# Kernel tuning notes

Measured on AMD Instinct MI355X. Metric: run time of the kernel, lower is better.

## Reference

```python
import jax, jax.numpy as jnp
import numpy as np
from jax.scipy.special import logsumexp

VOCAB, EMB, HID, K = 50000, 256, 512, 48
H = HID // 2
B, T = 64, 512


def setup_inputs() -> dict:
    key = jax.random.key(0)
    ks = jax.random.split(key, 15)
    f = lambda k, s: jax.random.normal(k, s, jnp.float32) * 0.1
    return {
        "x": jax.random.randint(ks[0], (B, T), 0, VOCAB),
        "tags": jax.random.randint(ks[1], (B, T), 0, K),
        "mask": jnp.ones((B, T), jnp.bool_),
        "emb": f(ks[2], (VOCAB, EMB)),
        "Wih_f": f(ks[3], (4 * H, EMB)),
        "Whh_f": f(ks[4], (4 * H, H)),
        "b_f": f(ks[5], (4 * H,)),
        "Wih_b": f(ks[6], (4 * H, EMB)),
        "Whh_b": f(ks[7], (4 * H, H)),
        "b_b": f(ks[8], (4 * H,)),
        "fc_W": f(ks[9], (K, HID)),
        "fc_b": f(ks[10], (K,)),
        "start_t": f(ks[11], (K,)),
        "end_t": f(ks[12], (K,)),
        "trans": f(ks[13], (K, K)),
    }


def _lstm_dir(xs, Wih, Whh, b, reverse):
    # xs: [S, N, E]; scan over axis 0 (PyTorch gate order i,f,g,o; bias = b_ih+b_hh)
    n = xs.shape[1]
    hdim = Whh.shape[1]

    def step(carry, x_t):
        h, c = carry
        gates = x_t @ Wih.T + h @ Whh.T + b
        i, fg, g, o = jnp.split(gates, 4, axis=-1)
        i = jax.nn.sigmoid(i)
        fg = jax.nn.sigmoid(fg)
        g = jnp.tanh(g)
        o = jax.nn.sigmoid(o)
        c = fg * c + i * g
        h = o * jnp.tanh(c)
        return (h, c), h

    init = (jnp.zeros((n, hdim), xs.dtype), jnp.zeros((n, hdim), xs.dtype))
    _, hs = jax.lax.scan(step, init, xs, reverse=reverse)
    return hs


def _crf_nll(emissions, tags, mask, start_t, end_t, trans):
    # torchcrf with batch_first=True, reduction='mean'; returns -llh.mean()
    em = jnp.transpose(emissions, (1, 0, 2))  # [T,B,K] time-major
    tg = tags.T                                # [T,B]
    m = mask.T.astype(em.dtype)                # [T,B]
    bidx = jnp.arange(em.shape[1])

    # numerator: score of the gold tag path
    emit = jnp.take_along_axis(em, tg[..., None], axis=-1)[..., 0]  # [T,B]
    tr = trans[tg[:-1], tg[1:]]                                      # [T-1,B]
    num = start_t[tg[0]] + emit[0] + jnp.sum((tr + emit[1:]) * m[1:], axis=0)
    last = (jnp.sum(mask, axis=1) - 1).astype(jnp.int32)             # [B]
    num = num + end_t[tg[last, bidx]]

    # denominator: forward algorithm (sequential logsumexp recurrence)
    def step(alpha, inp):
        e_t, m_t = inp
        nxt = logsumexp(alpha[:, :, None] + trans[None] + e_t[:, None, :], axis=1)
        return jnp.where(m_t[:, None] > 0, nxt, alpha), None

    alpha0 = start_t + em[0]                     # [B,K]
    alpha, _ = jax.lax.scan(step, alpha0, (em[1:], m[1:]))
    den = logsumexp(alpha + end_t, axis=-1)      # [B]
    return -jnp.mean(num - den)


def reference(x, tags, mask, emb, Wih_f, Whh_f, b_f, Wih_b, Whh_b, b_b, fc_W, fc_b, start_t, end_t, trans):
    table = emb.at[0].set(0.0)  # padding_idx=0 row is zero
    e = table[x]                # [B,T,EMB]
    # Faithful to source: batch-first embeds fed into a seq-first nn.LSTM,
    # so the recurrence runs over axis 0 (the data batch axis).
    h_f = _lstm_dir(e, Wih_f, Whh_f, b_f, False)
    h_b = _lstm_dir(e, Wih_b, Whh_b, b_b, True)
    lstm_out = jnp.concatenate([h_f, h_b], axis=-1)  # [B,T,HID]
    emissions = lstm_out @ fc_W.T + fc_b             # [B,T,K]
    return _crf_nll(emissions, tags, mask, start_t, end_t, trans)
```

## Files before the change

kernel.cpp:

```cpp
#include <hip/hip_runtime.h>
#include <hip/hip_bf16.h>

#define VOCAB 50000
#define EMBD 256
#define HIDD 512
#define KTAG 48
#define HD 256
#define BB 64
#define TT 512
#define GATES 1024

typedef __bf16 bf16x8 __attribute__((ext_vector_type(8)));
typedef float f32x4 __attribute__((ext_vector_type(4)));

#define GLDS16(gp, lp) __builtin_amdgcn_global_load_lds( \
    (const __attribute__((address_space(1))) void*)(gp), \
    (__attribute__((address_space(3))) void*)(lp), 16, 0, 0)

__device__ __forceinline__ f32x4 mfma16(bf16x8 a, bf16x8 b, f32x4 c){
  return __builtin_amdgcn_mfma_f32_16x16x32_bf16(a, b, c, 0, 0, 0);
}
__device__ __forceinline__ float fsig(float x){
  return __builtin_amdgcn_rcpf(1.0f + __expf(-x));
}
__device__ __forceinline__ float ftanh(float x){
  x = fminf(10.0f, fmaxf(-10.0f, x));
  float e = __expf(2.0f*x);
  return (e - 1.0f) * __builtin_amdgcn_rcpf(e + 1.0f);
}

__global__ __launch_bounds__(256) void convert_all(
    const float* emb, const float* wf, const float* wb,
    const float* uf, const float* ub, const float* fc,
    __bf16* o_emb, __bf16* o_wih, __bf16* o_uf, __bf16* o_ub, __bf16* o_fc){
  const long N_emb = (long)VOCAB*EMBD;
  const long N_w   = 1024L*256;
  const long N_fc  = 48L*512;
  const long total = N_emb + 4*N_w + N_fc;
  for (long i = (long)blockIdx.x*256 + threadIdx.x; i < total; i += (long)gridDim.x*256){
    long j = i;
    if (j < N_emb){ o_emb[j] = (__bf16)((j < EMBD) ? 0.0f : emb[j]); continue; }
    j -= N_emb;
    if (j < N_w){ o_wih[j] = (__bf16)wf[j]; continue; }
    j -= N_w;
    if (j < N_w){ o_wih[N_w + j] = (__bf16)wb[j]; continue; }
    j -= N_w;
    if (j < N_w){ o_uf[j] = (__bf16)uf[j]; continue; }
    j -= N_w;
    if (j < N_w){ o_ub[j] = (__bf16)ub[j]; continue; }
    j -= N_w;
    o_fc[j] = (__bf16)fc[j];
  }
}

__global__ __launch_bounds__(256) void gemm_pre(const int* x, const __bf16* embb,
                                                const __bf16* wih, __bf16* pre){
  __shared__ __attribute__((aligned(16))) __bf16 As[128*32];
  __shared__ __attribute__((aligned(16))) __bf16 Bs[128*32];
  const int bid = blockIdx.x;
  const int bm = bid >> 4, bn = bid & 15;
  const int m0 = bm*128, n0 = bn*128;
  const int tid = threadIdx.x, l = tid & 63, w = tid >> 6;
  const int lr = l & 15, lk = l >> 4;
  const int wm = w >> 1, wn = w & 1;
  f32x4 acc[4][4];
  #pragma unroll
  for (int a=0;a<4;a++) for (int b2=0;b2<4;b2++) acc[a][b2] = (f32x4){0.f,0.f,0.f,0.f};

  const __bf16* agp[2];
  const __bf16* bgp[2];
  #pragma unroll
  for (int c=0;c<2;c++){
    const int id = w*2 + c;
    const int slot = id*64 + l;
    const int r = slot >> 2, kk = (slot & 3)*8;
    const int idx = x[m0 + r];
    agp[c] = embb + (size_t)idx*EMBD + kk;
    bgp[c] = wih + (size_t)(n0 + r)*EMBD + kk;
  }

  for (int k0 = 0; k0 < EMBD; k0 += 32){
    __syncthreads();
    #pragma unroll
    for (int c=0;c<2;c++){
      const int id = w*2 + c;
      GLDS16(agp[c] + k0, As + id*512);
      GLDS16(bgp[c] + k0, Bs + id*512);
    }
    asm volatile("s_waitcnt vmcnt(0)" ::: "memory");
    __syncthreads();
    bf16x8 af[4], bfr[4];
    #pragma unroll
    for (int mt=0;mt<4;mt++) af[mt] = *(const bf16x8*)(&As[(wm*64 + mt*16 + lr)*32 + lk*8]);
    #pragma unroll
    for (int nt=0;nt<4;nt++) bfr[nt] = *(const bf16x8*)(&Bs[(wn*64 + nt*16 + lr)*32 + lk*8]);
    #pragma unroll
    for (int mt=0;mt<4;mt++)
      #pragma unroll
      for (int nt=0;nt<4;nt++)
        acc[mt][nt] = mfma16(af[mt], bfr[nt], acc[mt][nt]);
  }
  #pragma unroll
  for (int mt=0;mt<4;mt++)
    #pragma unroll
    for (int nt=0;nt<4;nt++)
      #pragma unroll
      for (int r=0;r<4;r++){
        const int row = m0 + wm*64 + mt*16 + lk*4 + r;
        const int col = n0 + wn*64 + nt*16 + lr;
        pre[(size_t)row*2048 + col] = (__bf16)acc[mt][nt][r];
      }
}

__global__ __launch_bounds__(512, 1) void lstm_rec(const __bf16* pre, const __bf16* whhF,
                                                   const __bf16* whhB, const float* biasF,
                                                   const float* biasB, __bf16* hcat){
  __shared__ __attribute__((aligned(16))) __bf16 hLDS[16*264];
  __shared__ __attribute__((aligned(16))) __bf16 preLDS[2][16*1032];
  const int bid = blockIdx.x;
  const int dir = bid & 1, tg = bid >> 1;
  const int t0 = tg*16;
  const int tid = threadIdx.x, l = tid & 63, w = tid >> 6;
  const int lr = l & 15, lk = l >> 4;
  const __bf16* whh = dir ? whhB : whhF;
  const float* bias = dir ? biasB : biasF;

  bf16x8 Bf[4][2][8];
  #pragma unroll
  for (int q=0;q<4;q++)
    #pragma unroll
    for (int j=0;j<2;j++)
      #pragma unroll
      for (int kt=0;kt<8;kt++){
        const int n = q*256 + w*32 + j*16 + lr;
        Bf[q][j][kt] = *(const bf16x8*)(&whh[(size_t)n*HD + kt*32 + lk*8]);
      }

  float brg[4][2];
  #pragma unroll
  for (int q=0;q<4;q++)
    #pragma unroll
    for (int j=0;j<2;j++)
      brg[q][j] = bias[q*256 + w*32 + j*16 + lr];

  float cst[2][4];
  #pragma unroll
  for (int j=0;j<2;j++)
    #pragma unroll
    for (int r=0;r<4;r++) cst[j][r] = 0.f;

  auto stage = [&](int buf, int bs){
    #pragma unroll
    for (int c2=0;c2<4;c2++){
      const int id = w*4 + c2;
      const int r = id >> 1, half = id & 1;
      const __bf16* g = pre + (size_t)(bs*TT + t0 + r)*2048 + dir*1024 + half*512 + l*8;
      GLDS16(g, &preLDS[buf][r*1032 + half*512]);
    }
  };

  stage(0, dir ? (BB-1) : 0);
  int prev_b = 0;

  #pragma unroll 1
  for (int s = 0; s < BB; s++){
    const int bs = dir ? (BB-1 - s) : s;
    const int buf = s & 1;
    asm volatile("s_waitcnt vmcnt(0)" ::: "memory");
    __syncthreads();
    if (s < BB-1) stage(buf^1, dir ? (BB-2 - s) : (s+1));
    if (s > 0){
      const int row = tid >> 5, ch = tid & 31;
      bf16x8 hv = *(const bf16x8*)(&hLDS[row*264 + ch*8]);
      *(bf16x8*)(&hcat[(size_t)(prev_b*TT + t0 + row)*HIDD + dir*HD + ch*8]) = hv;
    }
    f32x4 acc[4][2];
    #pragma unroll
    for (int q=0;q<4;q++)
      #pragma unroll
      for (int j=0;j<2;j++) acc[q][j] = (f32x4){0.f,0.f,0.f,0.f};
    if (s > 0){
      #pragma unroll
      for (int kt=0; kt<8; kt++){
        bf16x8 a = *(const bf16x8*)(&hLDS[lr*264 + kt*32 + lk*8]);
        #pragma unroll
        for (int q=0;q<4;q++)
          #pragma unroll
          for (int j=0;j<2;j++)
            acc[q][j] = mfma16(a, Bf[q][j][kt], acc[q][j]);
      }
    }
    __syncthreads();
    #pragma unroll
    for (int j=0;j<2;j++){
      const int colbase = w*32 + j*16 + lr;
      #pragma unroll
      for (int r=0;r<4;r++){
        const int row = lk*4 + r;
        float gi = acc[0][j][r] + (float)preLDS[buf][row*1032 +       colbase] + brg[0][j];
        float gf = acc[1][j][r] + (float)preLDS[buf][row*1032 + 256 + colbase] + brg[1][j];
        float gg = acc[2][j][r] + (float)preLDS[buf][row*1032 + 512 + colbase] + brg[2][j];
        float go = acc[3][j][r] + (float)preLDS[buf][row*1032 + 768 + colbase] + brg[3][j];
        float iv = fsig(gi), fv = fsig(gf), gv = ftanh(gg), ov = fsig(go);
        float cn = fv*cst[j][r] + iv*gv;
        cst[j][r] = cn;
        hLDS[row*264 + colbase] = (__bf16)(ov * ftanh(cn));
      }
    }
    prev_b = bs;
  }
  __syncthreads();
  {
    const int row = tid >> 5, ch = tid & 31;
    bf16x8 hv = *(const bf16x8*)(&hLDS[row*264 + ch*8]);
    *(bf16x8*)(&hcat[(size_t)(prev_b*TT + t0 + row)*HIDD + dir*HD + ch*8]) = hv;
  }
}

__global__ __launch_bounds__(256) void gemm_emis(const __bf16* hcat, const __bf16* fcw,
                                                 const float* fcb, float* emis){
  const int tid = threadIdx.x, l = tid & 63, w = tid >> 6;
  const int lr = l & 15, lk = l >> 4;
  const size_t m0 = (size_t)blockIdx.x*64 + w*16;
  f32x4 acc[3];
  #pragma unroll
  for (int nt=0;nt<3;nt++) acc[nt] = (f32x4){0.f,0.f,0.f,0.f};
  #pragma unroll
  for (int kt=0; kt<16; kt++){
    bf16x8 a = *(const bf16x8*)(&hcat[(m0 + lr)*HIDD + kt*32 + lk*8]);
    #pragma unroll
    for (int nt=0;nt<3;nt++){
      bf16x8 b = *(const bf16x8*)(&fcw[(size_t)(nt*16 + lr)*HIDD + kt*32 + lk*8]);
      acc[nt] = mfma16(a, b, acc[nt]);
    }
  }
  #pragma unroll
  for (int nt=0;nt<3;nt++){
    const int col = nt*16 + lr;
    const float bv = fcb[col];
    #pragma unroll
    for (int r=0;r<4;r++){
      const size_t row = m0 + lk*4 + r;
      emis[row*KTAG + col] = acc[nt][r] + bv;
    }
  }
}

__global__ __launch_bounds__(64) void crf_num(const int* tags, const float* emis,
                                              const float* trans, const float* start_t,
                                              const float* end_t, float* numv){
  const int b = blockIdx.x, l = threadIdx.x;
  float part = 0.f;
  for (int t = l; t < TT; t += 64){
    const int tg = tags[b*TT + t];
    const float e = emis[(size_t)(b*TT + t)*KTAG + tg];
    if (t > 0){
      const int tp = tags[b*TT + t - 1];
      part += trans[tp*KTAG + tg] + e;
    } else {
      part += start_t[tg] + e;
    }
  }
  #pragma unroll
  for (int off=32; off; off >>= 1) part += __shfl_down(part, off);
  if (l == 0){
    const int tl = tags[b*TT + TT - 1];
    numv[b] = part + end_t[tl];
  }
}

__global__ __launch_bounds__(64) void crf_den(const float* emis, const float* trans,
                                              const float* start_t, const float* end_t,
                                              float* denv){
  __shared__ float wlds[64];
  const int b = blockIdx.x, l = threadIdx.x;
  float E[48];
  #pragma unroll
  for (int j=0;j<48;j++) E[j] = (l < KTAG) ? __expf(trans[j*KTAG + l]) : 0.f;
  float alpha = (l < KTAG) ? (start_t[l] + emis[(size_t)(b*TT)*KTAG + l]) : -1e30f;

  float em_cur = (l < KTAG) ? emis[(size_t)(b*TT + 1)*KTAG + l] : 0.f;
  #pragma unroll 1
  for (int t = 1; t < TT; t++){
    float em_nxt = (l < KTAG && t < TT-1) ? emis[(size_t)(b*TT + t + 1)*KTAG + l] : 0.f;
    float m = alpha;
    #pragma unroll
    for (int off=32; off; off >>= 1) m = fmaxf(m, __shfl_xor(m, off));
    const float wv = __expf(alpha - m);
    wlds[l] = wv;
    asm volatile("s_waitcnt lgkmcnt(0)" ::: "memory");
    float s = 0.f;
    #pragma unroll
    for (int j=0;j<48;j+=4){
      const float4 w4 = *(const float4*)(&wlds[j]);
      s += w4.x*E[j] + w4.y*E[j+1] + w4.z*E[j+2] + w4.w*E[j+3];
    }
    asm volatile("" ::: "memory");
    alpha = (l < KTAG) ? (em_cur + m + __logf(s)) : -1e30f;
    em_cur = em_nxt;
  }
  float v = (l < KTAG) ? (alpha + end_t[l]) : -1e30f;
  float mf = v;
  #pragma unroll
  for (int off=32; off; off >>= 1) mf = fmaxf(mf, __shfl_xor(mf, off));
  float sv = __expf(v - mf);
  #pragma unroll
  for (int off=32; off; off >>= 1) sv += __shfl_xor(sv, off);
  if (l == 0) denv[b] = mf + __logf(sv);
}

__global__ __launch_bounds__(64) void finalize(const float* numv, const float* denv, float* out){
  const int l = threadIdx.x;
  float v = numv[l] - denv[l];
  #pragma unroll
  for (int off=32; off; off >>= 1) v += __shfl_down(v, off);
  if (l == 0) out[0] = -v * (1.0f/64.0f);
}

extern "C" void kernel_launch(void* const* d_in, const int* in_sizes, int n_in,
                              void* d_out, int out_size, void* d_ws, size_t ws_size,
                              hipStream_t stream){
  const int*   x     = (const int*)d_in[0];
  const int*   tags  = (const int*)d_in[1];
  const float* emb   = (const float*)d_in[3];
  const float* wih_f = (const float*)d_in[4];
  const float* whh_f = (const float*)d_in[5];
  const float* b_f   = (const float*)d_in[6];
  const float* wih_b = (const float*)d_in[7];
  const float* whh_b = (const float*)d_in[8];
  const float* b_b   = (const float*)d_in[9];
  const float* fc_W  = (const float*)d_in[10];
  const float* fc_b  = (const float*)d_in[11];
  const float* start_t = (const float*)d_in[12];
  const float* end_t   = (const float*)d_in[13];
  const float* trans   = (const float*)d_in[14];

  constexpr size_t SZ_EMBB = (size_t)VOCAB*EMBD*2;
  constexpr size_t SZ_WIH  = (size_t)2048*256*2;
  constexpr size_t SZ_WHH  = (size_t)1024*256*2;
  constexpr size_t SZ_FCW  = (size_t)48*512*2;
  constexpr size_t SZ_PRE  = (size_t)32768*2048*2;
  constexpr size_t SZ_HCAT = (size_t)32768*512*2;
  constexpr size_t SZ_EMIS = (size_t)32768*48*4;
  constexpr size_t TOTAL = SZ_EMBB + SZ_WIH + 2*SZ_WHH + SZ_FCW + SZ_PRE + SZ_HCAT + SZ_EMIS + 512;
  if (ws_size < TOTAL){ hipMemsetAsync(d_out, 0, sizeof(float), stream); return; }

  char* ws = (char*)d_ws;
  size_t off = 0;
  __bf16* embb  = (__bf16*)(ws + off); off += SZ_EMBB;
  __bf16* wihb  = (__bf16*)(ws + off); off += SZ_WIH;
  __bf16* whhfb = (__bf16*)(ws + off); off += SZ_WHH;
  __bf16* whhbb = (__bf16*)(ws + off); off += SZ_WHH;
  __bf16* fcwb  = (__bf16*)(ws + off); off += SZ_FCW;
  __bf16* pre   = (__bf16*)(ws + off); off += SZ_PRE;
  __bf16* hcat  = (__bf16*)(ws + off); off += SZ_HCAT;
  float*  emis  = (float*)(ws + off);  off += SZ_EMIS;
  float*  numv  = (float*)(ws + off);  off += 256;
  float*  denv  = (float*)(ws + off);

  convert_all<<<4096, 256, 0, stream>>>(emb, wih_f, wih_b, whh_f, whh_b, fc_W,
                                        embb, wihb, whhfb, whhbb, fcwb);
  gemm_pre<<<4096, 256, 0, stream>>>(x, embb, wihb, pre);
  lstm_rec<<<64, 512, 0, stream>>>(pre, whhfb, whhbb, b_f, b_b, hcat);
  gemm_emis<<<512, 256, 0, stream>>>(hcat, fcwb, fc_b, emis);
  crf_num<<<64, 64, 0, stream>>>(tags, emis, trans, start_t, end_t, numv);
  crf_den<<<64, 64, 0, stream>>>(emis, trans, start_t, end_t, denv);
  finalize<<<1, 64, 0, stream>>>(numv, denv, (float*)d_out);
}
```

Before: 1.005 ms.

## Split LSTM recurrence across blocks with atomic barriers and double-buffer GEMM

The LSTM recurrence moves from 64 blocks of 512 threads to 512 blocks of 128 threads. Each block owns a 32-column slice of the hidden state and converts its slice of Whh into swizzled LDS itself, so the separate Whh conversion goes away. The h state is exchanged through global memory, with per-step atomic counters acting as a cross-block barrier, which adds spin-wait and coherence overhead in exchange for many more CUs working on each step. Separately, the gemm_pre K-loop is double-buffered and the LSTM bias is folded into its epilogue. crf_den now recomputes the row max only every 8 steps and splits its dot-product accumulation across four sums.

```diff
diff --git a/kernel.cpp b/kernel.cpp
--- a/kernel.cpp
+++ b/kernel.cpp
@@ -30,13 +30,12 @@
 }
 
 __global__ __launch_bounds__(256) void convert_all(
-    const float* emb, const float* wf, const float* wb,
-    const float* uf, const float* ub, const float* fc,
-    __bf16* o_emb, __bf16* o_wih, __bf16* o_uf, __bf16* o_ub, __bf16* o_fc){
+    const float* emb, const float* wf, const float* wb, const float* fc,
+    __bf16* o_emb, __bf16* o_wih, __bf16* o_fc){
   const long N_emb = (long)VOCAB*EMBD;
   const long N_w   = 1024L*256;
   const long N_fc  = 48L*512;
-  const long total = N_emb + 4*N_w + N_fc;
+  const long total = N_emb + 2*N_w + N_fc;
   for (long i = (long)blockIdx.x*256 + threadIdx.x; i < total; i += (long)gridDim.x*256){
     long j = i;
     if (j < N_emb){ o_emb[j] = (__bf16)((j < EMBD) ? 0.0f : emb[j]); continue; }
@@ -45,18 +44,15 @@
     j -= N_w;
     if (j < N_w){ o_wih[N_w + j] = (__bf16)wb[j]; continue; }
     j -= N_w;
-    if (j < N_w){ o_uf[j] = (__bf16)uf[j]; continue; }
-    j -= N_w;
-    if (j < N_w){ o_ub[j] = (__bf16)ub[j]; continue; }
-    j -= N_w;
     o_fc[j] = (__bf16)fc[j];
   }
 }
 
 __global__ __launch_bounds__(256) void gemm_pre(const int* x, const __bf16* embb,
-                                                const __bf16* wih, __bf16* pre){
-  __shared__ __attribute__((aligned(16))) __bf16 As[128*32];
-  __shared__ __attribute__((aligned(16))) __bf16 Bs[128*32];
+                                                const __bf16* wih, const float* bf,
+                                                const float* bb2, __bf16* pre){
+  __shared__ __attribute__((aligned(16))) __bf16 As[2][128*32];
+  __shared__ __attribute__((aligned(16))) __bf16 Bs[2][128*32];
   const int bid = blockIdx.x;
   const int bm = bid >> 4, bn = bid & 15;
   const int m0 = bm*128, n0 = bn*128;
@@ -79,141 +75,154 @@
     bgp[c] = wih + (size_t)(n0 + r)*EMBD + kk;
   }
 
-  for (int k0 = 0; k0 < EMBD; k0 += 32){
-    __syncthreads();
+  auto stage = [&](int buf, int k0){
     #pragma unroll
     for (int c=0;c<2;c++){
       const int id = w*2 + c;
-      GLDS16(agp[c] + k0, As + id*512);
-      GLDS16(bgp[c] + k0, Bs + id*512);
-    }
+      GLDS16(agp[c] + k0, &As[buf][id*512]);
+      GLDS16(bgp[c] + k0, &Bs[buf][id*512]);
+    }
+  };
+
+  stage(0, 0);
+  asm volatile("s_waitcnt vmcnt(0)" ::: "memory");
+  __syncthreads();
+
+  int cur = 0;
+  #pragma unroll 1
+  for (int it = 0; it < 8; it++){
+    if (it < 7) stage(cur^1, (it+1)*32);
+    bf16x8 af[4], bfr[4];
+    #pragma unroll
+    for (int mt=0;mt<4;mt++) af[mt] = *(const bf16x8*)(&As[cur][(wm*64 + mt*16 + lr)*32 + lk*8]);
+    #pragma unroll
+    for (int nt=0;nt<4;nt++) bfr[nt] = *(const bf16x8*)(&Bs[cur][(wn*64 + nt*16 + lr)*32 + lk*8]);
+    #pragma unroll
+    for (int mt=0;mt<4;mt++)
+      #pragma unroll
+      for (int nt=0;nt<4;nt++)
+        acc[mt][nt] = mfma16(af[mt], bfr[nt], acc[mt][nt]);
     asm volatile("s_waitcnt vmcnt(0)" ::: "memory");
     __syncthreads();
-    bf16x8 af[4], bfr[4];
-    #pragma unroll
-    for (int mt=0;mt<4;mt++) af[mt] = *(const bf16x8*)(&As[(wm*64 + mt*16 + lr)*32 + lk*8]);
-    #pragma unroll
-    for (int nt=0;nt<4;nt++) bfr[nt] = *(const bf16x8*)(&Bs[(wn*64 + nt*16 + lr)*32 + lk*8]);
-    #pragma unroll
-    for (int mt=0;mt<4;mt++)
-      #pragma unroll
-      for (int nt=0;nt<4;nt++)
-        acc[mt][nt] = mfma16(af[mt], bfr[nt], acc[mt][nt]);
+    cur ^= 1;
   }
   #pragma unroll
   for (int mt=0;mt<4;mt++)
     #pragma unroll
-    for (int nt=0;nt<4;nt++)
+    for (int nt=0;nt<4;nt++){
+      const int col = n0 + wn*64 + nt*16 + lr;
+      const float bv = (col < GATES) ? bf[col] : bb2[col - GATES];
       #pragma unroll
       for (int r=0;r<4;r++){
         const int row = m0 + wm*64 + mt*16 + lk*4 + r;
-        const int col = n0 + wn*64 + nt*16 + lr;
-        pre[(size_t)row*2048 + col] = (__bf16)acc[mt][nt][r];
+        pre[(size_t)row*2048 + col] = (__bf16)(acc[mt][nt][r] + bv);
       }
-}
-
-__global__ __launch_bounds__(512, 1) void lstm_rec(const __bf16* pre, const __bf16* whhF,
-                                                   const __bf16* whhB, const float* biasF,
-                                                   const float* biasB, __bf16* hcat){
-  __shared__ __attribute__((aligned(16))) __bf16 hLDS[16*264];
-  __shared__ __attribute__((aligned(16))) __bf16 preLDS[2][16*1032];
+    }
+}
+
+__global__ __launch_bounds__(128) void lstm_rec(const float* whhF, const float* whhB,
+                                                const __bf16* pre, __bf16* hcat,
+                                                int* cnt){
+  __shared__ __attribute__((aligned(16))) unsigned char wsh[65536];
   const int bid = blockIdx.x;
-  const int dir = bid & 1, tg = bid >> 1;
-  const int t0 = tg*16;
+  const int cs  = bid >> 6;
+  const int gid = bid & 63;
+  const int dir = gid >> 5;
+  const int g   = gid & 31;
+  const int t0 = g*16, c0 = cs*32;
   const int tid = threadIdx.x, l = tid & 63, w = tid >> 6;
   const int lr = l & 15, lk = l >> 4;
-  const __bf16* whh = dir ? whhB : whhF;
-  const float* bias = dir ? biasB : biasF;
-
-  bf16x8 Bf[4][2][8];
-  #pragma unroll
-  for (int q=0;q<4;q++)
-    #pragma unroll
-    for (int j=0;j<2;j++)
-      #pragma unroll
-      for (int kt=0;kt<8;kt++){
-        const int n = q*256 + w*32 + j*16 + lr;
-        Bf[q][j][kt] = *(const bf16x8*)(&whh[(size_t)n*HD + kt*32 + lk*8]);
-      }
-
-  float brg[4][2];
-  #pragma unroll
-  for (int q=0;q<4;q++)
-    #pragma unroll
-    for (int j=0;j<2;j++)
-      brg[q][j] = bias[q*256 + w*32 + j*16 + lr];
-
-  float cst[2][4];
-  #pragma unroll
-  for (int j=0;j<2;j++)
-    #pragma unroll
-    for (int r=0;r<4;r++) cst[j][r] = 0.f;
-
-  auto stage = [&](int buf, int bs){
-    #pragma unroll
-    for (int c2=0;c2<4;c2++){
-      const int id = w*4 + c2;
-      const int r = id >> 1, half = id & 1;
-      const __bf16* g = pre + (size_t)(bs*TT + t0 + r)*2048 + dir*1024 + half*512 + l*8;
-      GLDS16(g, &preLDS[buf][r*1032 + half*512]);
-    }
-  };
-
-  stage(0, dir ? (BB-1) : 0);
-  int prev_b = 0;
+  const float* whh = dir ? whhB : whhF;
+
+  #pragma unroll 4
+  for (int p = 0; p < 64; p++){
+    const int e = p*512 + tid*4;
+    const int R = e >> 8, k = e & 255;
+    const int q = R >> 5, rr = R & 31;
+    const float4 v = *(const float4*)(whh + (size_t)(q*256 + c0 + rr)*HD + k);
+    union { __bf16 h[4]; unsigned long long u; } pk;
+    pk.h[0]=(__bf16)v.x; pk.h[1]=(__bf16)v.y; pk.h[2]=(__bf16)v.z; pk.h[3]=(__bf16)v.w;
+    const int byte = R*512 + ((k*2) ^ ((R&7)<<4));
+    *(unsigned long long*)(&wsh[byte]) = pk.u;
+  }
+  __syncthreads();
+
+  const int mycol = c0 + w*16 + lr;
+  float cstate[4] = {0.f,0.f,0.f,0.f};
+
+  float pv[4][4], pvn[4][4];
+  {
+    const int bs0 = dir ? (BB-1) : 0;
+    #pragma unroll
+    for (int q=0;q<4;q++)
+      #pragma unroll
+      for (int r=0;r<4;r++)
+        pv[q][r] = (float)pre[(size_t)(bs0*TT + t0 + lk*4 + r)*2048 + dir*GATES + q*256 + mycol];
+  }
 
   #pragma unroll 1
   for (int s = 0; s < BB; s++){
-    const int bs = dir ? (BB-1 - s) : s;
-    const int buf = s & 1;
-    asm volatile("s_waitcnt vmcnt(0)" ::: "memory");
-    __syncthreads();
-    if (s < BB-1) stage(buf^1, dir ? (BB-2 - s) : (s+1));
+    const int bs = dir ? (BB-1-s) : s;
+    f32x4 acc[4];
+    #pragma unroll
+    for (int q=0;q<4;q++) acc[q] = (f32x4){0.f,0.f,0.f,0.f};
+
     if (s > 0){
-      const int row = tid >> 5, ch = tid & 31;
-      bf16x8 hv = *(const bf16x8*)(&hLDS[row*264 + ch*8]);
-      *(bf16x8*)(&hcat[(size_t)(prev_b*TT + t0 + row)*HIDD + dir*HD + ch*8]) = hv;
-    }
-    f32x4 acc[4][2];
-    #pragma unroll
-    for (int q=0;q<4;q++)
-      #pragma unroll
-      for (int j=0;j<2;j++) acc[q][j] = (f32x4){0.f,0.f,0.f,0.f};
-    if (s > 0){
-      #pragma unroll
-      for (int kt=0; kt<8; kt++){
-        bf16x8 a = *(const bf16x8*)(&hLDS[lr*264 + kt*32 + lk*8]);
+      const int prev = dir ? (bs+1) : (bs-1);
+      const __bf16* hp = hcat + ((size_t)prev*TT + t0 + lr)*HIDD + dir*HD;
+      bf16x8 af[8];
+      #pragma unroll
+      for (int kt=0;kt<8;kt++){
+        const unsigned long long* pp = (const unsigned long long*)(hp + kt*32 + lk*8);
+        union { unsigned long long u[2]; bf16x8 v; } cv;
+        cv.u[0] = __hip_atomic_load(pp,     __ATOMIC_RELAXED, __HIP_MEMORY_SCOPE_AGENT);
+        cv.u[1] = __hip_atomic_load(pp + 1, __ATOMIC_RELAXED, __HIP_MEMORY_SCOPE_AGENT);
+        af[kt] = cv.v;
+      }
+      #pragma unroll
+      for (int kt=0;kt<8;kt++)
         #pragma unroll
-        for (int q=0;q<4;q++)
-          #pragma unroll
-          for (int j=0;j<2;j++)
-            acc[q][j] = mfma16(a, Bf[q][j][kt], acc[q][j]);
+        for (int q=0;q<4;q++){
+          const int R = q*32 + w*16 + lr;
+          const int byte = R*512 + ((kt*64 + lk*16) ^ ((R&7)<<4));
+          acc[q] = mfma16(af[kt], *(const bf16x8*)(&wsh[byte]), acc[q]);
+        }
+    }
+
+    #pragma unroll
+    for (int r=0;r<4;r++){
+      float gi = acc[0][r] + pv[0][r];
+      float gf = acc[1][r] + pv[1][r];
+      float gg = acc[2][r] + pv[2][r];
+      float go = acc[3][r] + pv[3][r];
+      float iv=fsig(gi), fv=fsig(gf), gv=ftanh(gg), ov=fsig(go);
+      float cn = fv*cstate[r] + iv*gv;
+      cstate[r] = cn;
+      hcat[((size_t)bs*TT + t0 + lk*4 + r)*HIDD + dir*HD + mycol] = (__bf16)(ov*ftanh(cn));
+    }
+
+    if (s < BB-1){
+      const int bsn = dir ? (bs-1) : (bs+1);
+      #pragma unroll
+      for (int q=0;q<4;q++)
+        #pragma unroll
+        for (int r=0;r<4;r++)
+          pvn[q][r] = (float)pre[(size_t)(bsn*TT + t0 + lk*4 + r)*2048 + dir*GATES + q*256 + mycol];
+
+      __threadfence();
+      __syncthreads();
+      if (tid == 0){
+        const int ci = gid*64 + s;
+        __hip_atomic_fetch_add(&cnt[ci], 1, __ATOMIC_RELEASE, __HIP_MEMORY_SCOPE_AGENT);
+        while (__hip_atomic_load(&cnt[ci], __ATOMIC_ACQUIRE, __HIP_MEMORY_SCOPE_AGENT) < 8)
+          __builtin_amdgcn_s_sleep(2);
       }
-    }
-    __syncthreads();
-    #pragma unroll
-    for (int j=0;j<2;j++){
-      const int colbase = w*32 + j*16 + lr;
-      #pragma unroll
-      for (int r=0;r<4;r++){
-        const int row = lk*4 + r;
-        float gi = acc[0][j][r] + (float)preLDS[buf][row*1032 +       colbase] + brg[0][j];
-        float gf = acc[1][j][r] + (float)preLDS[buf][row*1032 + 256 + colbase] + brg[1][j];
-        float gg = acc[2][j][r] + (float)preLDS[buf][row*1032 + 512 + colbase] + brg[2][j];
-        float go = acc[3][j][r] + (float)preLDS[buf][row*1032 + 768 + colbase] + brg[3][j];
-        float iv = fsig(gi), fv = fsig(gf), gv = ftanh(gg), ov = fsig(go);
-        float cn = fv*cst[j][r] + iv*gv;
-        cst[j][r] = cn;
-        hLDS[row*264 + colbase] = (__bf16)(ov * ftanh(cn));
-      }
-    }
-    prev_b = bs;
-  }
-  __syncthreads();
-  {
-    const int row = tid >> 5, ch = tid & 31;
-    bf16x8 hv = *(const bf16x8*)(&hLDS[row*264 + ch*8]);
-    *(bf16x8*)(&hcat[(size_t)(prev_b*TT + t0 + row)*HIDD + dir*HD + ch*8]) = hv;
+      __syncthreads();
+      #pragma unroll
+      for (int q=0;q<4;q++)
+        #pragma unroll
+        for (int r=0;r<4;r++) pv[q][r] = pvn[q][r];
+    }
   }
 }
 
@@ -278,24 +287,35 @@
   #pragma unroll
   for (int j=0;j<48;j++) E[j] = (l < KTAG) ? __expf(trans[j*KTAG + l]) : 0.f;
   float alpha = (l < KTAG) ? (start_t[l] + emis[(size_t)(b*TT)*KTAG + l]) : -1e30f;
+  float m = 0.f;
 
   float em_cur = (l < KTAG) ? emis[(size_t)(b*TT + 1)*KTAG + l] : 0.f;
   #pragma unroll 1
   for (int t = 1; t < TT; t++){
     float em_nxt = (l < KTAG && t < TT-1) ? emis[(size_t)(b*TT + t + 1)*KTAG + l] : 0.f;
-    float m = alpha;
-    #pragma unroll
-    for (int off=32; off; off >>= 1) m = fmaxf(m, __shfl_xor(m, off));
+    if (((t-1) & 7) == 0){
+      float mm = alpha;
+      #pragma unroll
+      for (int off=32; off; off >>= 1) mm = fmaxf(mm, __shfl_xor(mm, off));
+      m = mm;
+    }
     const float wv = __expf(alpha - m);
     wlds[l] = wv;
     asm volatile("s_waitcnt lgkmcnt(0)" ::: "memory");
-    float s = 0.f;
-    #pragma unroll
-    for (int j=0;j<48;j+=4){
-      const float4 w4 = *(const float4*)(&wlds[j]);
-      s += w4.x*E[j] + w4.y*E[j+1] + w4.z*E[j+2] + w4.w*E[j+3];
+    float s0=0.f, s1=0.f, s2=0.f, s3=0.f;
+    #pragma unroll
+    for (int j=0;j<48;j+=16){
+      const float4 wa = *(const float4*)(&wlds[j]);
+      const float4 wb = *(const float4*)(&wlds[j+4]);
+      const float4 wc = *(const float4*)(&wlds[j+8]);
+      const float4 wd = *(const float4*)(&wlds[j+12]);
+      s0 += wa.x*E[j]    + wa.y*E[j+1]  + wa.z*E[j+2]  + wa.w*E[j+3];
+      s1 += wb.x*E[j+4]  + wb.y*E[j+5]  + wb.z*E[j+6]  + wb.w*E[j+7];
+      s2 += wc.x*E[j+8]  + wc.y*E[j+9]  + wc.z*E[j+10] + wc.w*E[j+11];
+      s3 += wd.x*E[j+12] + wd.y*E[j+13] + wd.z*E[j+14] + wd.w*E[j+15];
     }
     asm volatile("" ::: "memory");
+    const float s = (s0 + s1) + (s2 + s3);
     alpha = (l < KTAG) ? (em_cur + m + __logf(s)) : -1e30f;
     em_cur = em_nxt;
   }
@@ -337,31 +357,30 @@
 
   constexpr size_t SZ_EMBB = (size_t)VOCAB*EMBD*2;
   constexpr size_t SZ_WIH  = (size_t)2048*256*2;
-  constexpr size_t SZ_WHH  = (size_t)1024*256*2;
   constexpr size_t SZ_FCW  = (size_t)48*512*2;
   constexpr size_t SZ_PRE  = (size_t)32768*2048*2;
   constexpr size_t SZ_HCAT = (size_t)32768*512*2;
   constexpr size_t SZ_EMIS = (size_t)32768*48*4;
-  constexpr size_t TOTAL = SZ_EMBB + SZ_WIH + 2*SZ_WHH + SZ_FCW + SZ_PRE + SZ_HCAT + SZ_EMIS + 512;
+  constexpr size_t SZ_CNT  = 4096*4;
+  constexpr size_t TOTAL = SZ_EMBB + SZ_WIH + SZ_FCW + SZ_PRE + SZ_HCAT + SZ_EMIS + 512 + SZ_CNT;
   if (ws_size < TOTAL){ hipMemsetAsync(d_out, 0, sizeof(float), stream); return; }
 
   char* ws = (char*)d_ws;
   size_t off = 0;
   __bf16* embb  = (__bf16*)(ws + off); off += SZ_EMBB;
   __bf16* wihb  = (__bf16*)(ws + off); off += SZ_WIH;
-  __bf16* whhfb = (__bf16*)(ws + off); off += SZ_WHH;
-  __bf16* whhbb = (__bf16*)(ws + off); off += SZ_WHH;
   __bf16* fcwb  = (__bf16*)(ws + off); off += SZ_FCW;
   __bf16* pre   = (__bf16*)(ws + off); off += SZ_PRE;
   __bf16* hcat  = (__bf16*)(ws + off); off += SZ_HCAT;
   float*  emis  = (float*)(ws + off);  off += SZ_EMIS;
   float*  numv  = (float*)(ws + off);  off += 256;
-  float*  denv  = (float*)(ws + off);
-
-  convert_all<<<4096, 256, 0, stream>>>(emb, wih_f, wih_b, whh_f, whh_b, fc_W,
-                                        embb, wihb, whhfb, whhbb, fcwb);
-  gemm_pre<<<4096, 256, 0, stream>>>(x, embb, wihb, pre);
-  lstm_rec<<<64, 512, 0, stream>>>(pre, whhfb, whhbb, b_f, b_b, hcat);
+  float*  denv  = (float*)(ws + off);  off += 256;
+  int*    cnt   = (int*)(ws + off);
+
+  hipMemsetAsync(cnt, 0, SZ_CNT, stream);
+  convert_all<<<2048, 256, 0, stream>>>(emb, wih_f, wih_b, fc_W, embb, wihb, fcwb);
+  gemm_pre<<<4096, 256, 0, stream>>>(x, embb, wihb, b_f, b_b, pre);
+  lstm_rec<<<512, 128, 0, stream>>>(whh_f, whh_b, pre, hcat, cnt);
   gemm_emis<<<512, 256, 0, stream>>>(hcat, fcwb, fc_b, emis);
   crf_num<<<64, 64, 0, stream>>>(tags, emis, trans, start_t, end_t, numv);
   crf_den<<<64, 64, 0, stream>>>(emis, trans, start_t, end_t, denv);
```

After: 3.308 ms. 229% more time.
